# Performance work log

Hardware: AMD Instinct MI355X
Metric: run time of the kernel (lower is better)

Reference implementation:

```python
import jax, jax.numpy as jnp
from jax import lax
import numpy as np

EPS = 1e-5  # BatchNorm eps (eval mode, fresh running stats: mean=0, var=1)

N, T, H, C = 16, 512, 64, 64
O, K, E = 64, 9, 256


def setup_inputs() -> dict:
    key = jax.random.key(0)
    ks = jax.random.split(key, 16)
    X = jax.random.normal(ks[0], (N, T, H, C), dtype=jnp.float32)
    edges = jax.random.randint(ks[1], (N, 2, E), 0, H, dtype=jnp.int64)
    # att1/att2: Conv2d(C,1,1) == dot over channels + bias
    w_att1 = jax.random.normal(ks[2], (C,), jnp.float32) * (1.0 / np.sqrt(C))
    b_att1 = jax.random.normal(ks[3], (), jnp.float32) * 0.01
    w_att2 = jax.random.normal(ks[4], (C,), jnp.float32) * (1.0 / np.sqrt(C))
    b_att2 = jax.random.normal(ks[5], (), jnp.float32) * 0.01
    # GCN linear
    W_lin = jax.random.normal(ks[6], (O, C), jnp.float32) * (1.0 / np.sqrt(C))
    b_lin = jax.random.normal(ks[7], (O,), jnp.float32) * 0.01
    # tcn: BN -> ReLU -> Conv2d(O,O,(K,1)) -> BN -> Dropout(eval=id)
    bn1_gamma = 1.0 + 0.1 * jax.random.normal(ks[8], (O,), jnp.float32)
    bn1_beta = 0.1 * jax.random.normal(ks[9], (O,), jnp.float32)
    W_tcn = jax.random.normal(ks[10], (O, O, K, 1), jnp.float32) * (1.0 / np.sqrt(O * K))
    b_tcn = jax.random.normal(ks[11], (O,), jnp.float32) * 0.01
    bn2_gamma = 1.0 + 0.1 * jax.random.normal(ks[12], (O,), jnp.float32)
    bn2_beta = 0.1 * jax.random.normal(ks[13], (O,), jnp.float32)
    return dict(X=X, edges=edges, w_att1=w_att1, b_att1=b_att1, w_att2=w_att2,
                b_att2=b_att2, W_lin=W_lin, b_lin=b_lin, bn1_gamma=bn1_gamma,
                bn1_beta=bn1_beta, W_tcn=W_tcn, b_tcn=b_tcn,
                bn2_gamma=bn2_gamma, bn2_beta=bn2_beta)


def _bn_eval(x, gamma, beta):
    # eval-mode BatchNorm2d with running_mean=0, running_var=1; x is (N, Cc, T, H)
    inv = gamma / jnp.sqrt(1.0 + EPS)
    return x * inv[None, :, None, None] + beta[None, :, None, None]


def _forward(X, edges, w_att1, b_att1, w_att2, b_att2, W_lin, b_lin,
             bn1_gamma, bn1_beta, W_tcn, b_tcn, bn2_gamma, bn2_beta):
    n, t, h, c = X.shape
    k = W_tcn.shape[2]
    # --- adjacency from edge lists (duplicates sum, as sparse_coo->to_dense) ---
    bidx = jnp.arange(n)[:, None]
    adj = jnp.zeros((n, h, h), X.dtype).at[bidx, edges[:, 0, :], edges[:, 1, :]].add(1.0)
    # --- attention: a1[n,t,h] + a2[n,t,h'], leaky_relu, softmax over h ---
    a1 = jnp.einsum('nthc,c->nth', X, w_att1) + b_att1
    a2 = jnp.einsum('nthc,c->nth', X, w_att2) + b_att2
    s = jax.nn.leaky_relu(a1[:, :, :, None] + a2[:, :, None, :], 0.01)  # (n,t,h,h')
    att = jax.nn.softmax(s, axis=2)  # softmax over h (dim=1 pre-permute)
    # --- GCN: einsum('nthh,ntho->ntho') only uses diag(adj@att + I) ---
    diag = jnp.einsum('nhk,ntkh->nth', adj, att) + 1.0
    support = jnp.einsum('nthc,oc->ntho', X, W_lin) + b_lin  # (n,t,h,O)
    g = diag[..., None] * support
    # --- tcn: BN -> ReLU -> temporal conv (K,1) -> BN -> Dropout(eval) ---
    y = jnp.transpose(g, (0, 3, 1, 2))  # (n,O,t,h)
    y = jax.nn.relu(_bn_eval(y, bn1_gamma, bn1_beta))
    pad = (k - 1) // 2
    y = lax.conv_general_dilated(y, W_tcn, window_strides=(1, 1),
                                 padding=[(pad, pad), (0, 0)])
    y = y + b_tcn[None, :, None, None]
    y = _bn_eval(y, bn2_gamma, bn2_beta)
    # --- residual (identity: in==out, stride=1) + relu ---
    y = y + jnp.transpose(X, (0, 3, 1, 2))
    return jnp.transpose(jax.nn.relu(y), (0, 2, 3, 1))  # (n,t,h,O)


def reference(X, edges, w_att1, b_att1, w_att2, b_att2, W_lin, b_lin,
              bn1_gamma, bn1_beta, W_tcn, b_tcn, bn2_gamma, bn2_beta):
    return _forward(X, edges, w_att1, b_att1, w_att2, b_att2, W_lin, b_lin,
                    bn1_gamma, bn1_beta, W_tcn, b_tcn, bn2_gamma, bn2_beta)
```

## Files before the change

### kernel.cpp

```cpp
#include <hip/hip_runtime.h>
#include <hip/hip_bf16.h>
#include <stdint.h>

#define NB 16
#define TT 512
#define HH 64
#define CC 64
#define OO 64
#define KK 9
#define EE 256

typedef float f32x4 __attribute__((ext_vector_type(4)));
typedef __bf16 bf16x8 __attribute__((ext_vector_type(8)));
typedef unsigned short u16;
typedef unsigned int u32;

__device__ __forceinline__ u16 f2bf(float f) {
    u32 u = __float_as_uint(f);
    u32 r = (u + 0x7fffu + ((u >> 16) & 1u)) >> 16;
    return (u16)r;
}

__global__ __launch_bounds__(256) void k_adj(const int* __restrict__ edges,
                                             float* __restrict__ adj) {
    __shared__ float a[64 * 64];
    const int n = blockIdx.x;
    for (int i = threadIdx.x; i < 4096; i += 256) a[i] = 0.f;
    __syncthreads();
    {
        int r = edges[n * 512 + threadIdx.x];
        int c = edges[n * 512 + 256 + threadIdx.x];
        atomicAdd(&a[r * 64 + c], 1.0f);
    }
    __syncthreads();
    for (int i = threadIdx.x; i < 4096; i += 256) adj[n * 4096 + i] = a[i];
}

__global__ __launch_bounds__(256) void k_pack(const float* __restrict__ Wlin,
                                              const float* __restrict__ Wtcn,
                                              u16* __restrict__ wlin_p,
                                              u16* __restrict__ wtcn_p) {
    int idx = blockIdx.x * 256 + threadIdx.x;
    if (idx < 4096) {
        int jj = idx & 7, l = (idx >> 3) & 63, j = (idx >> 9) & 3, s = idx >> 11;
        int o = j * 16 + (l & 15);
        int c = s * 32 + (l >> 4) * 8 + jj;
        wlin_p[idx] = f2bf(Wlin[o * 64 + c]);
    }
    int i2 = idx - 4096;
    if (i2 >= 0 && i2 < 36864) {
        int jj = i2 & 7, l = (i2 >> 3) & 63, j = (i2 >> 9) & 3, s = (i2 >> 11) & 1, kk = i2 >> 12;
        int o = j * 16 + (l & 15);
        int op = s * 32 + (l >> 4) * 8 + jj;
        wtcn_p[i2] = f2bf(Wtcn[(o * 64 + op) * 9 + kk]);
    }
}

__global__ __launch_bounds__(256) void k_attn_gcn(
    const float* __restrict__ X, const float* __restrict__ adj,
    const float* __restrict__ w1g, const float* __restrict__ b1g,
    const float* __restrict__ w2g, const float* __restrict__ b2g,
    const float* __restrict__ blin, const u16* __restrict__ wlin_p,
    const float* __restrict__ g1, const float* __restrict__ be1,
    u16* __restrict__ z) {
    __shared__ __align__(16) u16 Xbf[64 * 72];
    __shared__ __align__(16) float U[6336];
    __shared__ float A1[64], A2[64], DG[64];
    float* const adjs = U;
    float* const p1 = U + 4160;
    float* const p2 = U + 4160 + 1088;

    const int tid = threadIdx.x;
    const int n = blockIdx.x >> 9, t = blockIdx.x & 511;
    const float* Xrow = X + (size_t)(n * 512 + t) * 4096;

    {
        const int c4 = tid & 15;
        const int r0 = tid >> 4;
        float4 wv1 = *(const float4*)(w1g + c4 * 4);
        float4 wv2 = *(const float4*)(w2g + c4 * 4);
#pragma unroll
        for (int i = 0; i < 4; i++) {
            int h = r0 + 16 * i;
            float4 xv = *(const float4*)(Xrow + h * 64 + c4 * 4);
            p1[h * 17 + c4] = xv.x * wv1.x + xv.y * wv1.y + xv.z * wv1.z + xv.w * wv1.w;
            p2[h * 17 + c4] = xv.x * wv2.x + xv.y * wv2.y + xv.z * wv2.z + xv.w * wv2.w;
            uint2 pk;
            pk.x = (u32)f2bf(xv.x) | ((u32)f2bf(xv.y) << 16);
            pk.y = (u32)f2bf(xv.z) | ((u32)f2bf(xv.w) << 16);
            *(uint2*)(&Xbf[h * 72 + c4 * 4]) = pk;
        }
        const float* adjn = adj + n * 4096;
#pragma unroll
        for (int i = 0; i < 16; i++) {
            int idx = tid + 256 * i;
            adjs[(idx >> 6) * 65 + (idx & 63)] = adjn[idx];
        }
    }
    __syncthreads();

    if (tid < 64) {
        float s = 0.f;
#pragma unroll
        for (int i = 0; i < 16; i++) s += p1[tid * 17 + i];
        A1[tid] = s + b1g[0];
    } else if (tid < 128) {
        int h = tid - 64;
        float s = 0.f;
#pragma unroll
        for (int i = 0; i < 16; i++) s += p2[h * 17 + i];
        A2[h] = s + b2g[0];
    }
    __syncthreads();

    {
        int h = tid >> 2, p = tid & 3;
        float a2h = A2[h];
        float num = 0.f, den = 0.f;
#pragma unroll
        for (int i = 0; i < 16; i++) {
            int k = p * 16 + i;
            float sv = A1[k] + a2h;
            sv = sv > 0.f ? sv : 0.01f * sv;
            float e = __expf(sv);
            den += e;
            num += adjs[h * 65 + k] * e;
        }
        p1[h * 17 + p] = num;
        p2[h * 17 + p] = den;
    }
    __syncthreads();
    if (tid < 64) {
        float num = p1[tid * 17 + 0] + p1[tid * 17 + 1] + p1[tid * 17 + 2] + p1[tid * 17 + 3];
        float den = p2[tid * 17 + 0] + p2[tid * 17 + 1] + p2[tid * 17 + 2] + p2[tid * 17 + 3];
        DG[tid] = num / den + 1.0f;
    }
    __syncthreads();

    const int w = tid >> 6, l = tid & 63;
    const int col = l & 15, q = l >> 4;
    f32x4 zv = {0.f, 0.f, 0.f, 0.f};
    f32x4 acc[4] = {zv, zv, zv, zv};
#pragma unroll
    for (int s = 0; s < 2; s++) {
        bf16x8 a = *(const bf16x8*)(&Xbf[(16 * w + col) * 72 + s * 32 + q * 8]);
#pragma unroll
        for (int j = 0; j < 4; j++) {
            bf16x8 b = *(const bf16x8*)(&wlin_p[((s * 4 + j) * 64 + l) * 8]);
            acc[j] = __builtin_amdgcn_mfma_f32_16x16x32_bf16(a, b, acc[j], 0, 0, 0);
        }
    }

    const float rsf = 1.0f / sqrtf(1.0f + 1e-5f);
    u16* OT = (u16*)U;
#pragma unroll
    for (int j = 0; j < 4; j++) {
        int o = 16 * j + col;
        float s1 = g1[o] * rsf;
        float bb = be1[o];
        float bl = blin[o];
#pragma unroll
        for (int r = 0; r < 4; r++) {
            int h = 16 * w + q * 4 + r;
            float v = (acc[j][r] + bl) * DG[h] * s1 + bb;
            v = v > 0.f ? v : 0.f;
            OT[h * 72 + 16 * j + col] = f2bf(v);
        }
    }
    __syncthreads();
    {
        int h = tid >> 2, seg = tid & 3;
        u16* zrow = z + ((size_t)(n * 64 + h) * 512 + t) * 64;
        uint4 v0 = *(const uint4*)(&OT[h * 72 + seg * 16]);
        uint4 v1 = *(const uint4*)(&OT[h * 72 + seg * 16 + 8]);
        *(uint4*)(zrow + seg * 16) = v0;
        *(uint4*)(zrow + seg * 16 + 8) = v1;
    }
}

__global__ __launch_bounds__(256) void k_tcn(
    const u16* __restrict__ z, const u16* __restrict__ wtcn_p,
    const float* __restrict__ X, const float* __restrict__ btcn,
    const float* __restrict__ g2, const float* __restrict__ be2,
    float* __restrict__ out) {
    __shared__ __align__(16) u16 As[264 * 72];

    const int tid = threadIdx.x;
    const int bid = blockIdx.x;
    const int n = bid >> 7, h = (bid >> 1) & 63, tb = (bid & 1) * 256;
    const u16* zp = z + (size_t)(n * 64 + h) * 512 * 64;

#pragma unroll
    for (int i = 0; i < 9; i++) {
        int idx = tid + 256 * i;
        if (idx < 2112) {
            int r = idx >> 3, c8 = idx & 7;
            int tg = tb - 4 + r;
            uint4 v = make_uint4(0u, 0u, 0u, 0u);
            if (tg >= 0 && tg < 512) v = *(const uint4*)(zp + tg * 64 + c8 * 8);
            *(uint4*)(&As[r * 72 + c8 * 8]) = v;
        }
    }
    __syncthreads();

    const int w = tid >> 6, l = tid & 63;
    const int col = l & 15, q = l >> 4;
    f32x4 zv = {0.f, 0.f, 0.f, 0.f};
    f32x4 acc[4][4];
#pragma unroll
    for (int mt = 0; mt < 4; mt++)
#pragma unroll
        for (int j = 0; j < 4; j++) acc[mt][j] = zv;

    for (int kk = 0; kk < 9; kk++) {
#pragma unroll
        for (int s = 0; s < 2; s++) {
            bf16x8 b[4];
#pragma unroll
            for (int j = 0; j < 4; j++)
                b[j] = *(const bf16x8*)(&wtcn_p[(((kk * 2 + s) * 4 + j) * 64 + l) * 8]);
            bf16x8 a[4];
#pragma unroll
            for (int mt = 0; mt < 4; mt++) {
                int row = 64 * w + 16 * mt + col + kk;
                a[mt] = *(const bf16x8*)(&As[row * 72 + s * 32 + q * 8]);
            }
#pragma unroll
            for (int mt = 0; mt < 4; mt++)
#pragma unroll
                for (int j = 0; j < 4; j++)
                    acc[mt][j] = __builtin_amdgcn_mfma_f32_16x16x32_bf16(a[mt], b[j], acc[mt][j], 0, 0, 0);
        }
    }

    const float rsf = 1.0f / sqrtf(1.0f + 1e-5f);
    float s2[4], c2[4];
#pragma unroll
    for (int j = 0; j < 4; j++) {
        int o = 16 * j + col;
        float s = g2[o] * rsf;
        s2[j] = s;
        c2[j] = btcn[o] * s + be2[o];
    }
#pragma unroll
    for (int mt = 0; mt < 4; mt++) {
#pragma unroll
        for (int r = 0; r < 4; r++) {
            int tt = tb + 64 * w + 16 * mt + 4 * q + r;
#pragma unroll
            for (int j = 0; j < 4; j++) {
                int o = 16 * j + col;
                size_t off = ((size_t)(n * 512 + tt) * 64 + h) * 64 + o;
                float v = acc[mt][j][r] * s2[j] + c2[j] + X[off];
                out[off] = v > 0.f ? v : 0.f;
            }
        }
    }
}

extern "C" void kernel_launch(void* const* d_in, const int* in_sizes, int n_in,
                              void* d_out, int out_size, void* d_ws, size_t ws_size,
                              hipStream_t stream) {
    const float* X    = (const float*)d_in[0];
    const int*  edges = (const int*)d_in[1];
    const float* w1   = (const float*)d_in[2];
    const float* b1   = (const float*)d_in[3];
    const float* w2   = (const float*)d_in[4];
    const float* b2   = (const float*)d_in[5];
    const float* Wlin = (const float*)d_in[6];
    const float* blin = (const float*)d_in[7];
    const float* g1   = (const float*)d_in[8];
    const float* be1  = (const float*)d_in[9];
    const float* Wtcn = (const float*)d_in[10];
    const float* btcn = (const float*)d_in[11];
    const float* g2   = (const float*)d_in[12];
    const float* be2  = (const float*)d_in[13];
    float* out = (float*)d_out;

    char* ws = (char*)d_ws;
    float* adj    = (float*)ws;
    u16*   wlin_p = (u16*)(ws + 262144);
    u16*   wtcn_p = (u16*)(ws + 262144 + 8192);
    u16*   z      = (u16*)(ws + 262144 + 8192 + 73728);

    hipLaunchKernelGGL(k_adj, dim3(16), dim3(256), 0, stream, edges, adj);
    hipLaunchKernelGGL(k_pack, dim3(160), dim3(256), 0, stream, Wlin, Wtcn, wlin_p, wtcn_p);
    hipLaunchKernelGGL(k_attn_gcn, dim3(16 * 512), dim3(256), 0, stream,
                       X, adj, w1, b1, w2, b2, blin, wlin_p, g1, be1, z);
    hipLaunchKernelGGL(k_tcn, dim3(16 * 64 * 2), dim3(256), 0, stream,
                       z, wtcn_p, X, btcn, g2, be2, out);
}
```

Baseline: 330.5 us.

## Fuse GCN linear into TCN kernel, pass only diag between kernels

The attention kernel now writes only the per-(n,h,t) diagonal scale. The GCN linear projection, BN1 and ReLU are recomputed inside the temporal-conv kernel from X, including a 4-row halo on each side. This drops the bf16 intermediate z tensor (a write plus a read of about 64 MB) in exchange for some redundant halo GEMM work. The TCN kernel also uses smaller 128-timestep tiles, which means more blocks. X is read with a stride of 4096 floats per row, so each row load is only 256 bytes.

```diff
diff --git a/kernel.cpp b/kernel.cpp
--- a/kernel.cpp
+++ b/kernel.cpp
@@ -1,14 +1,6 @@
 #include <hip/hip_runtime.h>
 #include <hip/hip_bf16.h>
 #include <stdint.h>
-
-#define NB 16
-#define TT 512
-#define HH 64
-#define CC 64
-#define OO 64
-#define KK 9
-#define EE 256
 
 typedef float f32x4 __attribute__((ext_vector_type(4)));
 typedef __bf16 bf16x8 __attribute__((ext_vector_type(8)));
@@ -56,19 +48,14 @@
     }
 }
 
-__global__ __launch_bounds__(256) void k_attn_gcn(
+__global__ __launch_bounds__(256) void k_attn(
     const float* __restrict__ X, const float* __restrict__ adj,
     const float* __restrict__ w1g, const float* __restrict__ b1g,
     const float* __restrict__ w2g, const float* __restrict__ b2g,
-    const float* __restrict__ blin, const u16* __restrict__ wlin_p,
-    const float* __restrict__ g1, const float* __restrict__ be1,
-    u16* __restrict__ z) {
-    __shared__ __align__(16) u16 Xbf[64 * 72];
-    __shared__ __align__(16) float U[6336];
-    __shared__ float A1[64], A2[64], DG[64];
-    float* const adjs = U;
-    float* const p1 = U + 4160;
-    float* const p2 = U + 4160 + 1088;
+    float* __restrict__ diag) {
+    __shared__ float adjs[64 * 65];
+    __shared__ float p1[64 * 17], p2[64 * 17];
+    __shared__ float A1[64], A2[64];
 
     const int tid = threadIdx.x;
     const int n = blockIdx.x >> 9, t = blockIdx.x & 511;
@@ -85,10 +72,6 @@
             float4 xv = *(const float4*)(Xrow + h * 64 + c4 * 4);
             p1[h * 17 + c4] = xv.x * wv1.x + xv.y * wv1.y + xv.z * wv1.z + xv.w * wv1.w;
             p2[h * 17 + c4] = xv.x * wv2.x + xv.y * wv2.y + xv.z * wv2.z + xv.w * wv2.w;
-            uint2 pk;
-            pk.x = (u32)f2bf(xv.x) | ((u32)f2bf(xv.y) << 16);
-            pk.y = (u32)f2bf(xv.z) | ((u32)f2bf(xv.w) << 16);
-            *(uint2*)(&Xbf[h * 72 + c4 * 4]) = pk;
         }
         const float* adjn = adj + n * 4096;
 #pragma unroll
@@ -133,84 +116,83 @@
     if (tid < 64) {
         float num = p1[tid * 17 + 0] + p1[tid * 17 + 1] + p1[tid * 17 + 2] + p1[tid * 17 + 3];
         float den = p2[tid * 17 + 0] + p2[tid * 17 + 1] + p2[tid * 17 + 2] + p2[tid * 17 + 3];
-        DG[tid] = num / den + 1.0f;
+        diag[((size_t)(n * 64 + tid)) * 512 + t] = num / den + 1.0f;
+    }
+}
+
+__global__ __launch_bounds__(256) void k_gcn_tcn(
+    const float* __restrict__ X, const float* __restrict__ diag,
+    const u16* __restrict__ wlin_p, const float* __restrict__ blin,
+    const float* __restrict__ g1, const float* __restrict__ be1,
+    const u16* __restrict__ wtcn_p, const float* __restrict__ btcn,
+    const float* __restrict__ g2, const float* __restrict__ be2,
+    float* __restrict__ out) {
+    __shared__ __align__(16) u16 As[144 * 72];
+    __shared__ float DGs[144];
+
+    const int tid = threadIdx.x;
+    const int bid = blockIdx.x;
+    const int n = bid >> 8, h = (bid >> 2) & 63, tb = (bid & 3) * 128;
+    const float* Xbase = X + ((size_t)(n * 512) * 64 + h) * 64;
+
+#pragma unroll
+    for (int i = 0; i < 9; i++) {
+        int idx = tid + 256 * i;
+        int r = idx >> 4, c4 = idx & 15;
+        int tg = tb - 4 + r;
+        float4 xv = make_float4(0.f, 0.f, 0.f, 0.f);
+        if (tg >= 0 && tg < 512) xv = *(const float4*)(Xbase + (size_t)tg * 4096 + c4 * 4);
+        uint2 pk;
+        pk.x = (u32)f2bf(xv.x) | ((u32)f2bf(xv.y) << 16);
+        pk.y = (u32)f2bf(xv.z) | ((u32)f2bf(xv.w) << 16);
+        *(uint2*)(&As[r * 72 + c4 * 4]) = pk;
+    }
+    if (tid < 144) {
+        int tg = tb - 4 + tid;
+        DGs[tid] = (tg >= 0 && tg < 512) ? diag[((size_t)(n * 64 + h)) * 512 + tg] : 0.f;
     }
     __syncthreads();
 
     const int w = tid >> 6, l = tid & 63;
     const int col = l & 15, q = l >> 4;
-    f32x4 zv = {0.f, 0.f, 0.f, 0.f};
-    f32x4 acc[4] = {zv, zv, zv, zv};
-#pragma unroll
-    for (int s = 0; s < 2; s++) {
-        bf16x8 a = *(const bf16x8*)(&Xbf[(16 * w + col) * 72 + s * 32 + q * 8]);
+    const float rsf = 1.0f / sqrtf(1.0f + 1e-5f);
+    const f32x4 zv = {0.f, 0.f, 0.f, 0.f};
+
+    for (int mt = w; mt < 9; mt += 4) {
+        f32x4 acc[4] = {zv, zv, zv, zv};
+#pragma unroll
+        for (int s = 0; s < 2; s++) {
+            bf16x8 a = *(const bf16x8*)(&As[(16 * mt + col) * 72 + s * 32 + q * 8]);
+#pragma unroll
+            for (int j = 0; j < 4; j++) {
+                bf16x8 b = *(const bf16x8*)(&wlin_p[((s * 4 + j) * 64 + l) * 8]);
+                acc[j] = __builtin_amdgcn_mfma_f32_16x16x32_bf16(a, b, acc[j], 0, 0, 0);
+            }
+        }
 #pragma unroll
         for (int j = 0; j < 4; j++) {
-            bf16x8 b = *(const bf16x8*)(&wlin_p[((s * 4 + j) * 64 + l) * 8]);
-            acc[j] = __builtin_amdgcn_mfma_f32_16x16x32_bf16(a, b, acc[j], 0, 0, 0);
-        }
-    }
-
-    const float rsf = 1.0f / sqrtf(1.0f + 1e-5f);
-    u16* OT = (u16*)U;
-#pragma unroll
-    for (int j = 0; j < 4; j++) {
-        int o = 16 * j + col;
-        float s1 = g1[o] * rsf;
-        float bb = be1[o];
-        float bl = blin[o];
-#pragma unroll
-        for (int r = 0; r < 4; r++) {
-            int h = 16 * w + q * 4 + r;
-            float v = (acc[j][r] + bl) * DG[h] * s1 + bb;
-            v = v > 0.f ? v : 0.f;
-            OT[h * 72 + 16 * j + col] = f2bf(v);
-        }
-    }
-    __syncthreads();
-    {
-        int h = tid >> 2, seg = tid & 3;
-        u16* zrow = z + ((size_t)(n * 64 + h) * 512 + t) * 64;
-        uint4 v0 = *(const uint4*)(&OT[h * 72 + seg * 16]);
-        uint4 v1 = *(const uint4*)(&OT[h * 72 + seg * 16 + 8]);
-        *(uint4*)(zrow + seg * 16) = v0;
-        *(uint4*)(zrow + seg * 16 + 8) = v1;
-    }
-}
-
-__global__ __launch_bounds__(256) void k_tcn(
-    const u16* __restrict__ z, const u16* __restrict__ wtcn_p,
-    const float* __restrict__ X, const float* __restrict__ btcn,
-    const float* __restrict__ g2, const float* __restrict__ be2,
-    float* __restrict__ out) {
-    __shared__ __align__(16) u16 As[264 * 72];
-
-    const int tid = threadIdx.x;
-    const int bid = blockIdx.x;
-    const int n = bid >> 7, h = (bid >> 1) & 63, tb = (bid & 1) * 256;
-    const u16* zp = z + (size_t)(n * 64 + h) * 512 * 64;
-
-#pragma unroll
-    for (int i = 0; i < 9; i++) {
-        int idx = tid + 256 * i;
-        if (idx < 2112) {
-            int r = idx >> 3, c8 = idx & 7;
-            int tg = tb - 4 + r;
-            uint4 v = make_uint4(0u, 0u, 0u, 0u);
-            if (tg >= 0 && tg < 512) v = *(const uint4*)(zp + tg * 64 + c8 * 8);
-            *(uint4*)(&As[r * 72 + c8 * 8]) = v;
-        }
-    }
-    __syncthreads();
-
-    const int w = tid >> 6, l = tid & 63;
-    const int col = l & 15, q = l >> 4;
-    f32x4 zv = {0.f, 0.f, 0.f, 0.f};
-    f32x4 acc[4][4];
-#pragma unroll
-    for (int mt = 0; mt < 4; mt++)
-#pragma unroll
-        for (int j = 0; j < 4; j++) acc[mt][j] = zv;
+            int o = 16 * j + col;
+            float s1 = g1[o] * rsf;
+            float bb = be1[o];
+            float bl = blin[o];
+#pragma unroll
+            for (int rr = 0; rr < 4; rr++) {
+                int row = 16 * mt + q * 4 + rr;
+                int tg = tb - 4 + row;
+                float v = (acc[j][rr] + bl) * DGs[row] * s1 + bb;
+                v = v > 0.f ? v : 0.f;
+                if (tg < 0 || tg >= 512) v = 0.f;
+                As[row * 72 + o] = f2bf(v);
+            }
+        }
+    }
+    __syncthreads();
+
+    f32x4 acc2[2][4];
+#pragma unroll
+    for (int mt = 0; mt < 2; mt++)
+#pragma unroll
+        for (int j = 0; j < 4; j++) acc2[mt][j] = zv;
 
     for (int kk = 0; kk < 9; kk++) {
 #pragma unroll
@@ -219,21 +201,20 @@
 #pragma unroll
             for (int j = 0; j < 4; j++)
                 b[j] = *(const bf16x8*)(&wtcn_p[(((kk * 2 + s) * 4 + j) * 64 + l) * 8]);
-            bf16x8 a[4];
-#pragma unroll
-            for (int mt = 0; mt < 4; mt++) {
-                int row = 64 * w + 16 * mt + col + kk;
+            bf16x8 a[2];
+#pragma unroll
+            for (int mt = 0; mt < 2; mt++) {
+                int row = 32 * w + 16 * mt + col + kk;
                 a[mt] = *(const bf16x8*)(&As[row * 72 + s * 32 + q * 8]);
             }
 #pragma unroll
-            for (int mt = 0; mt < 4; mt++)
+            for (int mt = 0; mt < 2; mt++)
 #pragma unroll
                 for (int j = 0; j < 4; j++)
-                    acc[mt][j] = __builtin_amdgcn_mfma_f32_16x16x32_bf16(a[mt], b[j], acc[mt][j], 0, 0, 0);
-        }
-    }
-
-    const float rsf = 1.0f / sqrtf(1.0f + 1e-5f);
+                    acc2[mt][j] = __builtin_amdgcn_mfma_f32_16x16x32_bf16(a[mt], b[j], acc2[mt][j], 0, 0, 0);
+        }
+    }
+
     float s2[4], c2[4];
 #pragma unroll
     for (int j = 0; j < 4; j++) {
@@ -243,15 +224,15 @@
         c2[j] = btcn[o] * s + be2[o];
     }
 #pragma unroll
-    for (int mt = 0; mt < 4; mt++) {
-#pragma unroll
-        for (int r = 0; r < 4; r++) {
-            int tt = tb + 64 * w + 16 * mt + 4 * q + r;
+    for (int mt = 0; mt < 2; mt++) {
+#pragma unroll
+        for (int rr = 0; rr < 4; rr++) {
+            int tt = tb + 32 * w + 16 * mt + 4 * q + rr;
 #pragma unroll
             for (int j = 0; j < 4; j++) {
                 int o = 16 * j + col;
                 size_t off = ((size_t)(n * 512 + tt) * 64 + h) * 64 + o;
-                float v = acc[mt][j][r] * s2[j] + c2[j] + X[off];
+                float v = acc2[mt][j][rr] * s2[j] + c2[j] + X[off];
                 out[off] = v > 0.f ? v : 0.f;
             }
         }
@@ -281,12 +262,12 @@
     float* adj    = (float*)ws;
     u16*   wlin_p = (u16*)(ws + 262144);
     u16*   wtcn_p = (u16*)(ws + 262144 + 8192);
-    u16*   z      = (u16*)(ws + 262144 + 8192 + 73728);
+    float* diag   = (float*)(ws + 262144 + 8192 + 73728);
 
     hipLaunchKernelGGL(k_adj, dim3(16), dim3(256), 0, stream, edges, adj);
     hipLaunchKernelGGL(k_pack, dim3(160), dim3(256), 0, stream, Wlin, Wtcn, wlin_p, wtcn_p);
-    hipLaunchKernelGGL(k_attn_gcn, dim3(16 * 512), dim3(256), 0, stream,
-                       X, adj, w1, b1, w2, b2, blin, wlin_p, g1, be1, z);
-    hipLaunchKernelGGL(k_tcn, dim3(16 * 64 * 2), dim3(256), 0, stream,
-                       z, wtcn_p, X, btcn, g2, be2, out);
-}
+    hipLaunchKernelGGL(k_attn, dim3(16 * 512), dim3(256), 0, stream,
+                       X, adj, w1, b1, w2, b2, diag);
+    hipLaunchKernelGGL(k_gcn_tcn, dim3(16 * 64 * 4), dim3(256), 0, stream,
+                       X, diag, wlin_p, blin, g1, be1, wtcn_p, btcn, g2, be2, out);
+}
```

New measurement: 319.7 us. 1.03x faster.
